# Optimization experiments

Measured on AMD Instinct MI355X. Metric: run time of the kernel, lower is better.

## Reference

```python
import math
import jax, jax.numpy as jnp
from jax import lax
import numpy as np

SCORE_THR = 0.5
IOU_THR = 0.7
MIN_SIZE = 1.0
BBOX_CLIP = math.log(1000.0 / 16.0)

FEAT_SIZES = [100, 50, 25, 13, 7]
STRIDES = [8, 16, 32, 64, 128]
RATIOS = (0.5, 1.0, 2.0)
C = 256
A = 3
N = 2


def _make_priors(fs, stride):
    base = stride * 4.0
    ys, xs = np.meshgrid(np.arange(fs), np.arange(fs), indexing='ij')
    cx = (xs + 0.5) * stride
    cy = (ys + 0.5) * stride
    pri = []
    for r in RATIOS:
        w = base / np.sqrt(r)
        h = base * np.sqrt(r)
        pri.append(np.stack([cx - w / 2, cy - h / 2, cx + w / 2, cy + h / 2], axis=-1))
    pri = np.stack(pri, axis=2)  # (fs, fs, A, 4): H,W,A order matches permute/reshape
    return jnp.asarray(pri.reshape(-1, 4), dtype=jnp.float32)


def setup_inputs():
    key = jax.random.key(0)
    ks = jax.random.split(key, 8)
    inp = {}
    for i, fs in enumerate(FEAT_SIZES):
        inp[f'fmap{i}'] = jax.random.normal(jax.random.fold_in(ks[0], i), (N, C, fs, fs), dtype=jnp.float32)
        inp[f'priors{i}'] = _make_priors(fs, STRIDES[i])
    sc = 0.02
    inp['conv_w'] = jax.random.normal(ks[1], (C, C, 3, 3), jnp.float32) * sc
    inp['conv_b'] = jnp.zeros((C,), jnp.float32)
    inp['log_w'] = jax.random.normal(ks[2], (A, C, 1, 1), jnp.float32) * sc
    inp['log_b'] = jnp.zeros((A,), jnp.float32)
    inp['reg_w'] = jax.random.normal(ks[3], (A * 4, C, 1, 1), jnp.float32) * sc
    inp['reg_b'] = jnp.zeros((A * 4,), jnp.float32)
    inp['imsizes'] = jnp.full((N, 2), 800, dtype=jnp.int32)  # (h, w) per image
    inp['lvtop'] = 500
    inp['imtop'] = 100
    return inp


def _conv(x, w, b, pad):
    y = lax.conv_general_dilated(x, w, (1, 1), pad, dimension_numbers=('NCHW', 'OIHW', 'NCHW'))
    return y + b[None, :, None, None]


def _decode(reg, pri):
    pw = pri[..., 2] - pri[..., 0]
    ph = pri[..., 3] - pri[..., 1]
    pcx = pri[..., 0] + 0.5 * pw
    pcy = pri[..., 1] + 0.5 * ph
    dx, dy = reg[..., 0], reg[..., 1]
    dw = jnp.minimum(reg[..., 2], BBOX_CLIP)
    dh = jnp.minimum(reg[..., 3], BBOX_CLIP)
    cx = dx * pw + pcx
    cy = dy * ph + pcy
    w = jnp.exp(dw) * pw
    h = jnp.exp(dh) * ph
    return jnp.stack([cx - 0.5 * w, cy - 0.5 * h, cx + 0.5 * w, cy + 0.5 * h], axis=-1)


def _head(x, priors, conv_w, conv_b, log_w, log_b, reg_w, reg_b, lvtop):
    n = x.shape[0]
    h = jax.nn.relu(_conv(x, conv_w, conv_b, 'SAME'))
    reg = _conv(h, reg_w, reg_b, 'VALID').transpose(0, 2, 3, 1).reshape(n, -1, 4)
    log = _conv(h, log_w, log_b, 'VALID').transpose(0, 2, 3, 1).reshape(n, -1)
    k = min(lvtop, log.shape[1])
    vals, top = lax.top_k(log, k)                           # (n, k)
    reg = jnp.take_along_axis(reg, top[..., None], axis=1)  # (n, k, 4)
    pri = priors[top]                                       # (n, k, 4)
    return _decode(reg, pri), vals, k


def _box_iou(a, b):
    area_a = (a[:, 2] - a[:, 0]) * (a[:, 3] - a[:, 1])
    area_b = (b[:, 2] - b[:, 0]) * (b[:, 3] - b[:, 1])
    lt = jnp.maximum(a[:, None, :2], b[None, :, :2])
    rb = jnp.minimum(a[:, None, 2:], b[None, :, 2:])
    wh = jnp.clip(rb - lt, 0.0)
    inter = wh[..., 0] * wh[..., 1]
    return inter / (area_a[:, None] + area_b[None, :] - inter + 1e-9)


def _forward(fmaps, priors, conv_w, conv_b, log_w, log_b, reg_w, reg_b, imsizes, lvtop, imtop):
    tups = [_head(x, p, conv_w, conv_b, log_w, log_b, reg_w, reg_b, lvtop)
            for x, p in zip(fmaps, priors)]
    boxes = jnp.concatenate([t[0] for t in tups], axis=1)                 # (n, D, 4)
    obj = jax.nn.sigmoid(jnp.concatenate([t[1] for t in tups], axis=1))   # (n, D)
    lvlen = jnp.asarray([t[2] for t in tups])
    n, D = obj.shape
    boxes = boxes.reshape(-1, 4)
    obj = obj.reshape(-1)
    K = n * D
    imidx = jnp.arange(K) // D
    valid = obj >= SCORE_THR                                # score filter (masked, not nonzero)
    hw = imsizes[imidx].astype(jnp.float32)                 # (K, 2) = (h, w)
    x1 = jnp.clip(boxes[:, 0], 0.0, hw[:, 1])
    y1 = jnp.clip(boxes[:, 1], 0.0, hw[:, 0])
    x2 = jnp.clip(boxes[:, 2], 0.0, hw[:, 1])
    y2 = jnp.clip(boxes[:, 3], 0.0, hw[:, 0])
    boxes = jnp.stack([x1, y1, x2, y2], axis=-1)
    valid &= (x2 - x1 >= MIN_SIZE) & (y2 - y1 >= MIN_SIZE)  # remove_small
    lvidx = jnp.searchsorted(jnp.cumsum(lvlen), jnp.arange(K) % D, side='right')
    groups = imidx * 10 + lvidx
    scores = jnp.where(valid, obj, -jnp.inf)
    order = jnp.argsort(-scores)                            # global score order; groups gate suppression
    b, g, v, ii = boxes[order], groups[order], valid[order], imidx[order]
    iou = _box_iou(b, b)                                    # (K, K)
    ar = jnp.arange(K)
    def body(i, keep):
        sup = (iou[i] > IOU_THR) & (g == g[i]) & (ar > i)
        return jnp.where(keep[i], keep & ~sup, keep)
    keep = lax.fori_loop(0, K, body, v)                     # greedy batched NMS
    def select(i):
        m = keep & (ii == i)
        sel = jnp.argsort(~m)[:imtop]                       # stable: kept boxes in score order
        val = m[sel]
        bx = jnp.where(val[:, None], b[sel], 0.0)
        ix = jnp.where(val, i, -1)
        return bx, ix
    bx, ix = jax.vmap(select)(jnp.arange(n))
    return bx.reshape(n * imtop, 4), ix.reshape(n * imtop)


def reference(fmap0, fmap1, fmap2, fmap3, fmap4, priors0, priors1, priors2, priors3, priors4,
              conv_w, conv_b, log_w, log_b, reg_w, reg_b, imsizes, lvtop, imtop):
    return _forward([fmap0, fmap1, fmap2, fmap3, fmap4],
                    [priors0, priors1, priors2, priors3, priors4],
                    conv_w, conv_b, log_w, log_b, reg_w, reg_b, imsizes, lvtop, imtop)
```

## Files before the change

### kernel.cpp

```cpp
#include <hip/hip_runtime.h>
#include <math.h>


#define N_IMG 2
#define C_CH  256
#define D_PER 2147
#define K_TOT 4294
#define CONV_BLOCKS 1912
#define CPX 239

typedef double v4d __attribute__((ext_vector_type(4)));

__constant__ int c_Ml[5]     = {30000, 7500, 1875, 507, 147};
__constant__ int c_kl[5]     = {500, 500, 500, 500, 147};
__constant__ int c_logoff[5] = {0, 60000, 75000, 78750, 79764};
__constant__ int c_regoff[5] = {0, 240000, 300000, 315000, 319056};
__constant__ int c_fs[5]     = {100, 50, 25, 13, 7};
__constant__ int c_npt[5]    = {13, 7, 4, 2, 1};
__constant__ int c_E[5]      = {10000, 2500, 625, 169, 49};
__constant__ int c_cumbl[6]  = {0, 1352, 1744, 1872, 1904, 1912};
__constant__ int c_hcum[6]   = {0, 157, 197, 207, 210, 211};
__constant__ size_t c_hoff[5] = {0, 5120000, 6400000, 6720000, 6806528};

__global__ void transpose_w_kernel(const float* __restrict__ w,
                                   double* __restrict__ wT2) {
  int i = blockIdx.x * 256 + threadIdx.x;
  if (i >= 589824) return;
  int q = i % 2304;
  int slab = i / 2304;
  int cobi = slab >> 6, ch = slab & 63;
  int tap = q / 256;
  int rem = q % 256;
  int ci = rem >> 6, co = rem & 63;
  wT2[i] =
      (double)w[(size_t)(cobi * 64 + co) * 2304 + (ch * 4 + ci) * 9 + tap];
}

template <typename T>
__global__ __launch_bounds__(256) void conv_fused_kernel(
    const float* __restrict__ x0, const float* __restrict__ x1,
    const float* __restrict__ x2, const float* __restrict__ x3,
    const float* __restrict__ x4, const double* __restrict__ wT2,
    const float* __restrict__ bias, T* __restrict__ h) {
  __shared__ __align__(16) double s_in[2 * 480];
  int tid = threadIdx.x;
  int bid = (blockIdx.x & 7) * CPX + (blockIdx.x >> 3);
  int l = 0;
  while (bid >= c_cumbl[l + 1]) ++l;
  int r = bid - c_cumbl[l];
  int fs = c_fs[l], npt = c_npt[l];
  int tiles = npt * npt;
  int tile = r % tiles;
  int cn = r / tiles;
  int cobi = cn & 3, n = cn >> 2;
  int ptx = tile % npt, pty = tile / npt;
  int px0 = ptx * 8, py0 = pty * 8;
  int E = fs * fs;
  const float* xl;
  switch (l) {
    case 0: xl = x0; break;
    case 1: xl = x1; break;
    case 2: xl = x2; break;
    case 3: xl = x3; break;
    default: xl = x4; break;
  }
  const float* xn = xl + (size_t)n * C_CH * E;
  T* hl = h + c_hoff[l];

  int lane = tid & 63;
  int wv = tid >> 6;
  int lx = lane & 15;
  int lk = lane >> 4;

  double ind0 = (lk == 0) ? 1.0 : 0.0;
  v4d pr1 = __builtin_amdgcn_mfma_f64_16x16x4f64((double)lx, ind0,
                                                 (v4d)0.0, 0, 0, 0);
  v4d pr2 = __builtin_amdgcn_mfma_f64_16x16x4f64(ind0, (double)lx,
                                                 (v4d)0.0, 0, 0, 0);
  int coL[4], pxL[4];
#pragma unroll
  for (int q = 0; q < 4; ++q) {
    coL[q] = (int)pr1[q];
    pxL[q] = (int)pr2[q];
  }

  int in_dst[2], in_src[2];
#pragma unroll
  for (int it = 0; it < 2; ++it) {
    int idx = tid + it * 256;
    in_dst[it] = -1;
    in_src[it] = -1;
    if (idx < 400) {
      int ci = idx / 100, rr2 = idx % 100;
      int hy = rr2 / 10, hx = rr2 % 10;
      int gy = py0 - 1 + hy, gx = px0 - 1 + hx;
      in_dst[it] = ci * 120 + hy * 12 + hx;
      if (gy >= 0 && gy < fs && gx >= 0 && gx < fs)
        in_src[it] = ci * E + gy * fs + gx;
    }
  }

  int bOff[4];
#pragma unroll
  for (int p = 0; p < 4; ++p) {
    int pxidx = p * 16 + lx;
    bOff[p] = lk * 120 + (pxidx >> 3) * 12 + (pxidx & 7);
  }

  v4d acc[4];
#pragma unroll
  for (int p = 0; p < 4; ++p) acc[p] = (v4d)0.0;

  const double* wptr =
      wT2 + (size_t)cobi * 64 * 2304 + lk * 64 + wv * 16 + lx;

  double wcur[9], wnxt[9];
#pragma unroll
  for (int t = 0; t < 9; ++t) wcur[t] = wptr[t * 256];
  {
    float v0[2];
#pragma unroll
    for (int it = 0; it < 2; ++it)
      v0[it] = (in_dst[it] >= 0 && in_src[it] >= 0) ? xn[in_src[it]] : 0.f;
#pragma unroll
    for (int it = 0; it < 2; ++it)
      if (in_dst[it] >= 0) s_in[in_dst[it]] = (double)v0[it];
  }
  __syncthreads();

  for (int ch = 0; ch < 64; ++ch) {
    int buf = ch & 1;
    bool more = (ch + 1 < 64);
    float inx[2];
    if (more) {
      const float* xc1 = xn + (size_t)(ch + 1) * 4 * E;
#pragma unroll
      for (int it = 0; it < 2; ++it)
        inx[it] =
            (in_dst[it] >= 0 && in_src[it] >= 0) ? xc1[in_src[it]] : 0.f;
      const double* wn = wptr + 2304;
#pragma unroll
      for (int t = 0; t < 9; ++t) wnxt[t] = wn[t * 256];
    }
    const double* bb = s_in + buf * 480;
#pragma unroll
    for (int ky = 0; ky < 3; ++ky) {
#pragma unroll
      for (int kx = 0; kx < 3; ++kx) {
        int tap = ky * 3 + kx;
        double av = wcur[tap];
        int boff = ky * 12 + kx;
#pragma unroll
        for (int p = 0; p < 4; ++p) {
          double bv = bb[bOff[p] + boff];
          acc[p] = __builtin_amdgcn_mfma_f64_16x16x4f64(av, bv, acc[p],
                                                        0, 0, 0);
        }
      }
    }
    if (more) {
      double* db = s_in + (buf ^ 1) * 480;
#pragma unroll
      for (int it = 0; it < 2; ++it)
        if (in_dst[it] >= 0) db[in_dst[it]] = (double)inx[it];
#pragma unroll
      for (int t = 0; t < 9; ++t) wcur[t] = wnxt[t];
    }
    __syncthreads();
    wptr += 2304;
  }

#pragma unroll
  for (int p = 0; p < 4; ++p) {
#pragma unroll
    for (int rr2 = 0; rr2 < 4; ++rr2) {
      int pxidx = p * 16 + pxL[rr2];
      int gy = py0 + (pxidx >> 3), gx = px0 + (pxidx & 7);
      int co = cobi * 64 + wv * 16 + coL[rr2];
      if (gy < fs && gx < fs) {
        double v = acc[p][rr2] + (double)bias[co];
        hl[((size_t)n * C_CH + co) * E + gy * fs + gx] = (T)fmax(v, 0.0);
      }
    }
  }
}

template <typename T>
__global__ __launch_bounds__(256) void heads_fused_kernel(
    const T* __restrict__ h, const float* __restrict__ logw,
    const float* __restrict__ logb, const float* __restrict__ regw,
    const float* __restrict__ regb, double* __restrict__ logits,
    double* __restrict__ regs) {
  __shared__ float s_wh[256][16];
  __shared__ double s_red[4][15][64];
  int tid = threadIdx.x;
  int n = blockIdx.y;
  int cidx = blockIdx.x;
  int l = 0;
  while (cidx >= c_hcum[l + 1]) ++l;
  int chunk = cidx - c_hcum[l];
  int E = c_E[l];
  int px0 = chunk * 64;
  const T* hl = h + c_hoff[l];
  double* logits_l = logits + c_logoff[l];
  double* regs_l = regs + c_regoff[l];

  for (int idx = tid; idx < 4096; idx += 256) {
    int c = idx >> 4, j = idx & 15;
    float v = 0.f;
    if (j < 3) v = logw[j * 256 + c];
    else if (j < 15) v = regw[(j - 3) * 256 + c];
    s_wh[c][j] = v;
  }
  __syncthreads();

  int p = tid & 63, c4 = tid >> 6;
  int pix = px0 + p;
  bool act = pix < E;
  double acc[15];
#pragma unroll
  for (int j = 0; j < 15; j++) acc[j] = 0.0;
  if (act) {
    const T* hp = hl + ((size_t)n * C_CH + c4 * 64) * E + pix;
    for (int cc = 0; cc < 64; ++cc) {
      double hv = (double)hp[(size_t)cc * E];
      const float* wr = &s_wh[c4 * 64 + cc][0];
#pragma unroll
      for (int j = 0; j < 15; j++)
        acc[j] = fma((double)wr[j], hv, acc[j]);
    }
  }
#pragma unroll
  for (int j = 0; j < 15; j++) s_red[c4][j][p] = acc[j];
  __syncthreads();
  if (act) {
    int M = E * 3;
    for (int j = c4; j < 15; j += 4) {
      double v = s_red[0][j][p] + s_red[1][j][p] + s_red[2][j][p] +
                 s_red[3][j][p];
      if (j < 3) {
        logits_l[(size_t)n * M + pix * 3 + j] = v + (double)logb[j];
      } else {
        int rj = j - 3, a = rj >> 2, coord = rj & 3;
        regs_l[((size_t)n * M + pix * 3 + a) * 4 + coord] =
            v + (double)regb[rj];
      }
    }
  }
}

__device__ __forceinline__ unsigned long long d2key(double v) {
  unsigned long long ub = (unsigned long long)__double_as_longlong(v);
  return (ub >> 63) ? ~ub : (ub | 0x8000000000000000ull);
}

#define TK_CH 30
union TkShared {
  struct {
    int histw[16][256];
    int hist[256];
    int sgt[1024];
    int seq[1024];
  } a;
  struct {
    unsigned long long u[512];
    int idx[512];
    int keep[512];
    int ps[512];
    int m;
    double bx[512][4];
    unsigned long long mask[512][8];
  } b;
};

__global__ __launch_bounds__(1024) void topk_nms_kernel(
    const double* __restrict__ logits, const double* __restrict__ regs,
    const float* __restrict__ p0, const float* __restrict__ p1,
    const float* __restrict__ p2, const float* __restrict__ p3,
    const float* __restrict__ p4, const int* __restrict__ imsizes,
    double* __restrict__ g_box, unsigned long long* __restrict__ g_u,
    int* __restrict__ g_cnt) {
  __shared__ TkShared sh;
  __shared__ int s_sel[512];
  __shared__ unsigned long long s_prefix;
  __shared__ int s_r;
  int bid = blockIdx.x;
  int n = bid / 5, l = bid % 5;
  int M = c_Ml[l], k = c_kl[l];
  const double* lg = logits + c_logoff[l] + (size_t)n * M;
  int tid = threadIdx.x;
  if (tid == 0) { s_prefix = 0ull; s_r = k; }

  int chunk = (M + 1023) >> 10;
  int i0 = tid * chunk, i1 = min(M, i0 + chunk);
  int cnt = i1 - i0;
  if (cnt < 0) cnt = 0;
  unsigned long long kv[TK_CH];
#pragma unroll
  for (int q = 0; q < TK_CH; q++)
    if (q < cnt) kv[q] = d2key(lg[i0 + q]);
  int wid = tid >> 6;
  __syncthreads();

  for (int pass = 0; pass < 8; ++pass) {
    int shift = 56 - pass * 8;
    for (int i = tid; i < 4096; i += 1024) ((int*)sh.a.histw)[i] = 0;
    __syncthreads();
    unsigned long long pfx = s_prefix;
    int rr = s_r;
#pragma unroll
    for (int q = 0; q < TK_CH; q++) {
      if (q < cnt) {
        unsigned long long u = kv[q];
        if (pass == 0 || (u >> (shift + 8)) == pfx)
          atomicAdd(&sh.a.histw[wid][(int)((u >> shift) & 255ull)], 1);
      }
    }
    __syncthreads();
    if (tid < 256) {
      int s = 0;
#pragma unroll
      for (int w = 0; w < 16; w++) s += sh.a.histw[w][tid];
      sh.a.hist[tid] = s;
    }
    __syncthreads();
    if (tid == 0) {
      int s = 0, beta = 0;
      for (int b = 255; b >= 0; --b) {
        if (s + sh.a.hist[b] >= rr) { beta = b; break; }
        s += sh.a.hist[b];
      }
      s_prefix = (pfx << 8) | (unsigned long long)beta;
      s_r = rr - s;
    }
    __syncthreads();
  }
  unsigned long long T = s_prefix;
  int need = s_r;
  int cgt = 0, ceq = 0;
#pragma unroll
  for (int q = 0; q < TK_CH; q++) {
    if (q < cnt) {
      cgt += (kv[q] > T);
      ceq += (kv[q] == T);
    }
  }
  sh.a.sgt[tid] = cgt;
  sh.a.seq[tid] = ceq;
  __syncthreads();
  for (int o = 1; o < 1024; o <<= 1) {
    int a = (tid >= o) ? sh.a.sgt[tid - o] : 0;
    int b2 = (tid >= o) ? sh.a.seq[tid - o] : 0;
    __syncthreads();
    sh.a.sgt[tid] += a;
    sh.a.seq[tid] += b2;
    __syncthreads();
  }
  int gt_total = sh.a.sgt[1023];
  int pg = sh.a.sgt[tid] - cgt, pe = sh.a.seq[tid] - ceq;
#pragma unroll
  for (int q = 0; q < TK_CH; q++) {
    if (q < cnt) {
      unsigned long long u = kv[q];
      if (u > T) {
        s_sel[pg++] = i0 + q;
      } else if (u == T) {
        if (pe < need) s_sel[gt_total + pe] = i0 + q;
        pe++;
      }
    }
  }
  __syncthreads();

  const float* pp;
  switch (l) {
    case 0: pp = p0; break;
    case 1: pp = p1; break;
    case 2: pp = p2; break;
    case 3: pp = p3; break;
    default: pp = p4; break;
  }
  const double* regs_l = regs + c_regoff[l];
  double imh = (double)imsizes[n * 2 + 0], imw = (double)imsizes[n * 2 + 1];
  const double BCLIP = 4.1351665567423560;
  if (tid < 512) {
    unsigned long long key = 0ull;
    sh.b.idx[tid] = tid;
    sh.b.keep[tid] = 0;
    if (tid < k) {
      int aidx = s_sel[tid];
      double lv = lg[aidx];
      double obj = 1.0 / (1.0 + exp(-lv));
      const double* rp = regs_l + ((size_t)n * M + aidx) * 4;
      const float* pr = pp + (size_t)aidx * 4;
      double px1 = pr[0], py1 = pr[1], px2 = pr[2], py2 = pr[3];
      double pw = px2 - px1, ph = py2 - py1;
      double pcx = px1 + 0.5 * pw, pcy = py1 + 0.5 * ph;
      double dx = rp[0], dy = rp[1];
      double dw = fmin(rp[2], BCLIP), dh = fmin(rp[3], BCLIP);
      double cx = dx * pw + pcx, cy = dy * ph + pcy;
      double w = exp(dw) * pw, hh = exp(dh) * ph;
      double x1 = cx - 0.5 * w, y1 = cy - 0.5 * hh;
      double x2 = cx + 0.5 * w, y2 = cy + 0.5 * hh;
      x1 = fmin(fmax(x1, 0.0), imw);
      x2 = fmin(fmax(x2, 0.0), imw);
      y1 = fmin(fmax(y1, 0.0), imh);
      y2 = fmin(fmax(y2, 0.0), imh);
      bool valid = (obj >= 0.5) && ((x2 - x1) >= 1.0) && ((y2 - y1) >= 1.0);
      sh.b.bx[tid][0] = x1;
      sh.b.bx[tid][1] = y1;
      sh.b.bx[tid][2] = x2;
      sh.b.bx[tid][3] = y2;
      if (valid) key = d2key(obj);
    }
    sh.b.u[tid] = key;
  }
  if (tid == 0) sh.b.m = 0;
  __syncthreads();

  for (int kk = 2; kk <= 512; kk <<= 1) {
    for (int j = kk >> 1; j > 0; j >>= 1) {
      if (tid < 512) {
        int i = tid, ixj = i ^ j;
        if (ixj > i) {
          unsigned long long ua = sh.b.u[i], ub = sh.b.u[ixj];
          int ia = sh.b.idx[i], ib = sh.b.idx[ixj];
          bool up = ((i & kk) == 0);
          bool aAfterB = (ua < ub) || (ua == ub && ia > ib);
          bool sw = up ? aAfterB : !aAfterB && (ua != ub || ia != ib);
          if (sw) {
            sh.b.u[i] = ub; sh.b.u[ixj] = ua;
            sh.b.idx[i] = ib; sh.b.idx[ixj] = ia;
          }
        }
      }
      __syncthreads();
    }
  }
  if (tid < 512) {
    if (sh.b.u[tid] != 0ull && (tid == 511 || sh.b.u[tid + 1] == 0ull))
      sh.b.m = tid + 1;
  }
  __syncthreads();
  int m = sh.b.m;

  if (tid < 512 && tid < m) {
    int i = tid;
    const double* A = sh.b.bx[sh.b.idx[i]];
    double ax1 = A[0], ay1 = A[1], ax2 = A[2], ay2 = A[3];
    double areaA = (ax2 - ax1) * (ay2 - ay1);
    unsigned long long row[8] = {0, 0, 0, 0, 0, 0, 0, 0};
    for (int j = i + 1; j < m; ++j) {
      const double* B = sh.b.bx[sh.b.idx[j]];
      double bx1 = B[0], by1 = B[1], bx2 = B[2], by2 = B[3];
      double areaB = (bx2 - bx1) * (by2 - by1);
      double lx = fmax(ax1, bx1), ly = fmax(ay1, by1);
      double rx = fmin(ax2, bx2), ry = fmin(ay2, by2);
      double iw = fmax(rx - lx, 0.0), ih = fmax(ry - ly, 0.0);
      double inter = iw * ih;
      double iou = inter / (areaA + areaB - inter + 1e-9);
      if (iou > 0.7) row[j >> 6] |= (1ull << (j & 63));
    }
#pragma unroll
    for (int w2 = 0; w2 < 8; ++w2) sh.b.mask[i][w2] = row[w2];
  }
  __syncthreads();

  if (tid == 0) {
    unsigned long long remv[8] = {0, 0, 0, 0, 0, 0, 0, 0};
    for (int i = 0; i < m; ++i) {
      if (!((remv[i >> 6] >> (i & 63)) & 1ull)) {
        sh.b.keep[i] = 1;
#pragma unroll
        for (int w2 = 0; w2 < 8; ++w2) remv[w2] |= sh.b.mask[i][w2];
      }
    }
  }
  __syncthreads();

  if (tid < 512) sh.b.ps[tid] = sh.b.keep[tid];
  __syncthreads();
  for (int o = 1; o < 512; o <<= 1) {
    int v = 0;
    if (tid < 512 && tid >= o) v = sh.b.ps[tid - o];
    __syncthreads();
    if (tid < 512) sh.b.ps[tid] += v;
    __syncthreads();
  }
  if (tid < 512 && sh.b.keep[tid]) {
    int pos = sh.b.ps[tid] - 1;
    const double* B = sh.b.bx[sh.b.idx[tid]];
    size_t gbase = (size_t)bid * 512 + pos;
#pragma unroll
    for (int q = 0; q < 4; q++) g_box[gbase * 4 + q] = B[q];
    g_u[gbase] = sh.b.u[tid];
  }
  if (tid == 0) g_cnt[bid] = (m > 0) ? sh.b.ps[511] : 0;
}

__global__ __launch_bounds__(256) void select_kernel(
    const double* __restrict__ g_box, const unsigned long long* __restrict__ g_u,
    const int* __restrict__ g_cnt, float* __restrict__ out) {
  __shared__ unsigned long long s_u[5][512];
  __shared__ int s_pick[100];
  __shared__ int s_total;
  int n = blockIdx.x;
  int tid = threadIdx.x;
  int cnts[5];
#pragma unroll
  for (int l = 0; l < 5; l++) cnts[l] = g_cnt[n * 5 + l];
  for (int idx = tid; idx < 5 * 512; idx += 256) {
    int l = idx >> 9, r = idx & 511;
    s_u[l][r] = (r < cnts[l]) ? g_u[(size_t)(n * 5 + l) * 512 + r] : 0ull;
  }
  __syncthreads();
  if (tid == 0) {
    int hd[5] = {0, 0, 0, 0, 0};
    int t = 0;
    while (t < 100) {
      int bl = -1;
      unsigned long long bu = 0ull;
      for (int l = 0; l < 5; l++) {
        if (hd[l] < cnts[l] && s_u[l][hd[l]] > bu) {
          bu = s_u[l][hd[l]];
          bl = l;
        }
      }
      if (bl < 0) break;
      s_pick[t++] = bl * 512 + hd[bl];
      hd[bl]++;
    }
    s_total = t;
  }
  __syncthreads();
  int total = s_total;
  for (int t = tid; t < 100; t += 256) {
    if (t < total) {
      int pk = s_pick[t];
      int l = pk >> 9, r = pk & 511;
      size_t gbase = (size_t)(n * 5 + l) * 512 + r;
#pragma unroll
      for (int q = 0; q < 4; q++)
        out[(n * 100 + t) * 4 + q] = (float)g_box[gbase * 4 + q];
      out[800 + n * 100 + t] = (float)n;
    } else {
#pragma unroll
      for (int q = 0; q < 4; q++) out[(n * 100 + t) * 4 + q] = 0.0f;
      out[800 + n * 100 + t] = -1.0f;
    }
  }
}

extern "C" void kernel_launch(void* const* d_in, const int* in_sizes, int n_in,
                              void* d_out, int out_size, void* d_ws,
                              size_t ws_size, hipStream_t stream) {
  (void)in_sizes; (void)n_in; (void)out_size;
  const float* fmap[5];
  const float* priors[5];
  for (int l = 0; l < 5; l++) {
    fmap[l] = (const float*)d_in[2 * l];
    priors[l] = (const float*)d_in[2 * l + 1];
  }
  const float* conv_w = (const float*)d_in[10];
  const float* conv_b = (const float*)d_in[11];
  const float* log_w = (const float*)d_in[12];
  const float* log_b = (const float*)d_in[13];
  const float* reg_w = (const float*)d_in[14];
  const float* reg_b = (const float*)d_in[15];
  const int* imsizes = (const int*)d_in[16];
  float* out = (float*)d_out;

  bool f64h = ws_size >= (size_t)66000000;

  char* base = (char*)d_ws;
  size_t off = 0;
  auto alloc = [&](size_t bytes) -> void* {
    off = (off + 255) & ~(size_t)255;
    void* p = base + off;
    off += bytes;
    return p;
  };
  double* wT2 = (double*)alloc(589824ull * 8);
  void* hraw = alloc(6831616ull * (f64h ? 8 : 4));
  double* logits = (double*)alloc(80058ull * 8);
  double* regs = (double*)alloc(320232ull * 8);
  double* g_box = (double*)alloc(10ull * 512 * 4 * 8);
  unsigned long long* g_u = (unsigned long long*)alloc(10ull * 512 * 8);
  int* g_cnt = (int*)alloc(10 * 4);

  transpose_w_kernel<<<2304, 256, 0, stream>>>(conv_w, wT2);

  if (f64h) {
    conv_fused_kernel<double><<<CONV_BLOCKS, 256, 0, stream>>>(
        fmap[0], fmap[1], fmap[2], fmap[3], fmap[4], wT2, conv_b,
        (double*)hraw);
    heads_fused_kernel<double><<<dim3(211, 2), 256, 0, stream>>>(
        (double*)hraw, log_w, log_b, reg_w, reg_b, logits, regs);
  } else {
    conv_fused_kernel<float><<<CONV_BLOCKS, 256, 0, stream>>>(
        fmap[0], fmap[1], fmap[2], fmap[3], fmap[4], wT2, conv_b,
        (float*)hraw);
    heads_fused_kernel<float><<<dim3(211, 2), 256, 0, stream>>>(
        (float*)hraw, log_w, log_b, reg_w, reg_b, logits, regs);
  }
  topk_nms_kernel<<<10, 1024, 0, stream>>>(
      logits, regs, priors[0], priors[1], priors[2], priors[3], priors[4],
      imsizes, g_box, g_u, g_cnt);
  select_kernel<<<2, 256, 0, stream>>>(g_box, g_u, g_cnt, out);
}
```

Measured before the change: 1.035 ms.

## Process eight input channels per conv iteration and tile weight transpose via LDS

The conv loop now stages eight input channels per iteration instead of four, so there are half as many barriers and double-buffer swaps. The weight prefetch for the next step covers two channel groups. The weight transpose kernel now stages one slab in shared memory so its global writes are contiguous, using one block per slab. The cost is more registers for the doubled weight and input prefetch arrays, which may lower occupancy.

```diff
diff --git a/kernel.cpp b/kernel.cpp
--- a/kernel.cpp
+++ b/kernel.cpp
@@ -22,18 +22,23 @@
 __constant__ int c_hcum[6]   = {0, 157, 197, 207, 210, 211};
 __constant__ size_t c_hoff[5] = {0, 5120000, 6400000, 6720000, 6806528};
 
-__global__ void transpose_w_kernel(const float* __restrict__ w,
-                                   double* __restrict__ wT2) {
-  int i = blockIdx.x * 256 + threadIdx.x;
-  if (i >= 589824) return;
-  int q = i % 2304;
-  int slab = i / 2304;
-  int cobi = slab >> 6, ch = slab & 63;
-  int tap = q / 256;
-  int rem = q % 256;
-  int ci = rem >> 6, co = rem & 63;
-  wT2[i] =
-      (double)w[(size_t)(cobi * 64 + co) * 2304 + (ch * 4 + ci) * 9 + tap];
+__global__ __launch_bounds__(256) void transpose_w_kernel(
+    const float* __restrict__ w, double* __restrict__ wT2) {
+  __shared__ double s_t[2304];
+  int slab = blockIdx.x;
+  int cobi = slab >> 6, ch4 = slab & 63;
+  int t = threadIdx.x;
+  int co_l = t >> 2, ci = t & 3;
+  const float* src =
+      w + (size_t)(cobi * 64 + co_l) * 2304 + (ch4 * 4 + ci) * 9;
+#pragma unroll
+  for (int tap = 0; tap < 9; ++tap)
+    s_t[tap * 256 + ci * 64 + co_l] = (double)src[tap];
+  __syncthreads();
+  double* dst = wT2 + (size_t)slab * 2304 + t * 9;
+  const double* s = s_t + t * 9;
+#pragma unroll
+  for (int j = 0; j < 9; ++j) dst[j] = s[j];
 }
 
 template <typename T>
@@ -42,7 +47,7 @@
     const float* __restrict__ x2, const float* __restrict__ x3,
     const float* __restrict__ x4, const double* __restrict__ wT2,
     const float* __restrict__ bias, T* __restrict__ h) {
-  __shared__ __align__(16) double s_in[2 * 480];
+  __shared__ __align__(16) double s_in[2][960];
   int tid = threadIdx.x;
   int bid = (blockIdx.x & 7) * CPX + (blockIdx.x >> 3);
   int l = 0;
@@ -84,13 +89,13 @@
     pxL[q] = (int)pr2[q];
   }
 
-  int in_dst[2], in_src[2];
-#pragma unroll
-  for (int it = 0; it < 2; ++it) {
+  int in_dst[4], in_src[4];
+#pragma unroll
+  for (int it = 0; it < 4; ++it) {
     int idx = tid + it * 256;
     in_dst[it] = -1;
     in_src[it] = -1;
-    if (idx < 400) {
+    if (idx < 800) {
       int ci = idx / 100, rr2 = idx % 100;
       int hy = rr2 / 10, hx = rr2 % 10;
       int gy = py0 - 1 + hy, gx = px0 - 1 + hx;
@@ -114,60 +119,78 @@
   const double* wptr =
       wT2 + (size_t)cobi * 64 * 2304 + lk * 64 + wv * 16 + lx;
 
-  double wcur[9], wnxt[9];
-#pragma unroll
-  for (int t = 0; t < 9; ++t) wcur[t] = wptr[t * 256];
+  double wcur[18], wnxt[18];
+#pragma unroll
+  for (int t = 0; t < 9; ++t) {
+    wcur[t] = wptr[t * 256];
+    wcur[9 + t] = wptr[2304 + t * 256];
+  }
   {
-    float v0[2];
-#pragma unroll
-    for (int it = 0; it < 2; ++it)
+    float v0[4];
+#pragma unroll
+    for (int it = 0; it < 4; ++it)
       v0[it] = (in_dst[it] >= 0 && in_src[it] >= 0) ? xn[in_src[it]] : 0.f;
 #pragma unroll
-    for (int it = 0; it < 2; ++it)
-      if (in_dst[it] >= 0) s_in[in_dst[it]] = (double)v0[it];
-  }
-  __syncthreads();
-
-  for (int ch = 0; ch < 64; ++ch) {
-    int buf = ch & 1;
-    bool more = (ch + 1 < 64);
-    float inx[2];
+    for (int it = 0; it < 4; ++it)
+      if (in_dst[it] >= 0) s_in[0][in_dst[it]] = (double)v0[it];
+  }
+  __syncthreads();
+
+  for (int it = 0; it < 32; ++it) {
+    int buf = it & 1;
+    bool more = (it + 1 < 32);
+    float inx[4];
     if (more) {
-      const float* xc1 = xn + (size_t)(ch + 1) * 4 * E;
-#pragma unroll
-      for (int it = 0; it < 2; ++it)
-        inx[it] =
-            (in_dst[it] >= 0 && in_src[it] >= 0) ? xc1[in_src[it]] : 0.f;
-      const double* wn = wptr + 2304;
-#pragma unroll
-      for (int t = 0; t < 9; ++t) wnxt[t] = wn[t * 256];
-    }
-    const double* bb = s_in + buf * 480;
+      const float* xc1 = xn + (size_t)(it + 1) * 8 * E;
+#pragma unroll
+      for (int s = 0; s < 4; ++s)
+        inx[s] = (in_dst[s] >= 0 && in_src[s] >= 0) ? xc1[in_src[s]] : 0.f;
+      const double* wn = wptr + (size_t)(it + 1) * 4608;
+#pragma unroll
+      for (int t = 0; t < 9; ++t) {
+        wnxt[t] = wn[t * 256];
+        wnxt[9 + t] = wn[2304 + t * 256];
+      }
+    }
+    const double* bbA = s_in[buf];
+    const double* bbB = s_in[buf] + 480;
 #pragma unroll
     for (int ky = 0; ky < 3; ++ky) {
 #pragma unroll
       for (int kx = 0; kx < 3; ++kx) {
         int tap = ky * 3 + kx;
-        double av = wcur[tap];
         int boff = ky * 12 + kx;
+        double avA = wcur[tap];
 #pragma unroll
         for (int p = 0; p < 4; ++p) {
-          double bv = bb[bOff[p] + boff];
-          acc[p] = __builtin_amdgcn_mfma_f64_16x16x4f64(av, bv, acc[p],
-                                                        0, 0, 0);
+          acc[p] = __builtin_amdgcn_mfma_f64_16x16x4f64(
+              avA, bbA[bOff[p] + boff], acc[p], 0, 0, 0);
         }
       }
     }
+#pragma unroll
+    for (int ky = 0; ky < 3; ++ky) {
+#pragma unroll
+      for (int kx = 0; kx < 3; ++kx) {
+        int tap = ky * 3 + kx;
+        int boff = ky * 12 + kx;
+        double avB = wcur[9 + tap];
+#pragma unroll
+        for (int p = 0; p < 4; ++p) {
+          acc[p] = __builtin_amdgcn_mfma_f64_16x16x4f64(
+              avB, bbB[bOff[p] + boff], acc[p], 0, 0, 0);
+        }
+      }
+    }
     if (more) {
-      double* db = s_in + (buf ^ 1) * 480;
-#pragma unroll
-      for (int it = 0; it < 2; ++it)
-        if (in_dst[it] >= 0) db[in_dst[it]] = (double)inx[it];
-#pragma unroll
-      for (int t = 0; t < 9; ++t) wcur[t] = wnxt[t];
-    }
-    __syncthreads();
-    wptr += 2304;
+      double* db = s_in[buf ^ 1];
+#pragma unroll
+      for (int s = 0; s < 4; ++s)
+        if (in_dst[s] >= 0) db[in_dst[s]] = (double)inx[s];
+#pragma unroll
+      for (int t = 0; t < 18; ++t) wcur[t] = wnxt[t];
+    }
+    __syncthreads();
   }
 
 #pragma unroll
@@ -588,7 +611,7 @@
   unsigned long long* g_u = (unsigned long long*)alloc(10ull * 512 * 8);
   int* g_cnt = (int*)alloc(10 * 4);
 
-  transpose_w_kernel<<<2304, 256, 0, stream>>>(conv_w, wT2);
+  transpose_w_kernel<<<256, 256, 0, stream>>>(conv_w, wT2);
 
   if (f64h) {
     conv_fused_kernel<double><<<CONV_BLOCKS, 256, 0, stream>>>(
```

Result: faster. 1.004 ms (-2.9%).
